# Performance work log

Measured on AMD Instinct MI355X. Metric: run time of the kernel, lower is better.

## Reference

```python
import jax, jax.numpy as jnp
import numpy as np

N = 100000   # nodes
E = 1600000  # edges
HID = 128    # hidden_dim
H = 8        # heads
C = HID // H # head_dim = out_channels per head


def setup_inputs() -> dict:
    key = jax.random.key(0)
    ks = jax.random.split(key, 10)
    x = jax.random.normal(ks[0], (N, HID), jnp.float32)
    edge_index = jax.random.randint(ks[1], (2, E), 0, N, dtype=jnp.int64)
    edge_attr = jax.random.uniform(ks[2], (E,), jnp.float32)
    # GATConv params (lin_src == lin_dst shared since in_channels is int)
    W = jax.random.normal(ks[3], (HID, H * C), jnp.float32) / np.sqrt(HID)
    att_src = jax.random.normal(ks[4], (H, C), jnp.float32) / np.sqrt(C)
    att_dst = jax.random.normal(ks[5], (H, C), jnp.float32) / np.sqrt(C)
    # lin_edge: Linear(edge_dim=1, H*C, bias=False) -> weight [H*C, 1] stored as [H, C]
    w_edge = jax.random.normal(ks[6], (H, C), jnp.float32)
    att_edge = jax.random.normal(ks[7], (H, C), jnp.float32) / np.sqrt(C)
    bias = jnp.zeros((H * C,), jnp.float32)
    gamma = jnp.ones((HID,), jnp.float32)
    beta = jnp.zeros((HID,), jnp.float32)
    return dict(x=x, edge_index=edge_index, edge_attr=edge_attr, W=W,
                att_src=att_src, att_dst=att_dst, w_edge=w_edge,
                att_edge=att_edge, bias=bias, gamma=gamma, beta=beta)


def reference(x, edge_index, edge_attr, W, att_src, att_dst, w_edge, att_edge, bias, gamma, beta):
    n = x.shape[0]
    src, dst = edge_index[0], edge_index[1]
    # add_self_loops with fill_value='mean': loop edge_attr = per-dst-node mean of edge_attr
    ones = jnp.ones_like(edge_attr)
    deg = jax.ops.segment_sum(ones, dst, num_segments=n)
    loop_attr = jax.ops.segment_sum(edge_attr, dst, num_segments=n) / jnp.maximum(deg, 1.0)
    ar = jnp.arange(n, dtype=src.dtype)
    src = jnp.concatenate([src, ar])
    dst = jnp.concatenate([dst, ar])
    ea = jnp.concatenate([edge_attr, loop_attr])  # [E+N]

    h = (x @ W).reshape(n, H, C)                  # [N,H,C]
    a_src = (h * att_src).sum(-1)                 # [N,H]
    a_dst = (h * att_dst).sum(-1)                 # [N,H]
    # edge_dim=1: alpha_edge = <lin_edge(ea), att_edge> = ea * sum(w_edge*att_edge)
    w_e = (w_edge * att_edge).sum(-1)             # [H]
    alpha = a_src[src] + a_dst[dst] + ea[:, None] * w_e  # [E+N, H]
    alpha = jax.nn.leaky_relu(alpha, 0.2)
    # segment softmax over incoming edges of each dst node (all nodes have a self-loop)
    m = jax.ops.segment_max(alpha, dst, num_segments=n)      # [N,H]
    ex = jnp.exp(alpha - m[dst])
    denom = jax.ops.segment_sum(ex, dst, num_segments=n)     # [N,H]
    p = ex / (denom[dst] + 1e-16)
    # scatter-aggregate weighted messages, concat heads, bias
    out = jax.ops.segment_sum(p[:, :, None] * h[src], dst, num_segments=n)
    out = out.reshape(n, H * C) + bias
    # residual + LayerNorm + ReLU
    y = out + x
    mu = y.mean(-1, keepdims=True)
    var = ((y - mu) ** 2).mean(-1, keepdims=True)
    y = (y - mu) * jax.lax.rsqrt(var + 1e-5) * gamma + beta
    return jax.nn.relu(y)
```

## Files before the change

### kernel.cpp

```cpp
#include <hip/hip_runtime.h>
#include <math.h>

#define HID 128
#define HEADS 8
#define CDIM 16
#define NB1 256

typedef short bf8 __attribute__((ext_vector_type(8)));
typedef float f32x4 __attribute__((ext_vector_type(4)));

__device__ __forceinline__ unsigned short f2bf(float f) {
    unsigned u = __float_as_uint(f);
    unsigned r = (u + 0x7fffu + ((u >> 16) & 1u)) >> 16;
    return (unsigned short)r;
}
__device__ __forceinline__ float bf2f(unsigned short u) {
    return __uint_as_float(((unsigned)u) << 16);
}

__global__ __launch_bounds__(256) void k_tw(const float* __restrict__ W,
                                            unsigned short* __restrict__ Wt) {
    int idx = blockIdx.x * 256 + threadIdx.x;
    int j = idx >> 7, k = idx & 127;
    Wt[idx] = f2bf(W[k * HID + j]);
}

__global__ __launch_bounds__(256) void k_hist(const int* __restrict__ dst,
                                              int* __restrict__ cntmat,
                                              int E, int per, int nbkt) {
    __shared__ int h[256];
    int t = threadIdx.x;
    h[t] = 0;
    __syncthreads();
    int b0 = blockIdx.x * per;
    int b1 = min(b0 + per, E);
    for (int e = b0 + t; e < b1; e += 256)
        atomicAdd(&h[dst[e] >> 9], 1);
    __syncthreads();
    if (t < nbkt) cntmat[t * NB1 + blockIdx.x] = h[t];
}

__global__ __launch_bounds__(256) void kscanA(const int* __restrict__ in,
                                              int* __restrict__ tmp,
                                              int* __restrict__ bsum, int M) {
    __shared__ int lds[256];
    int t = threadIdx.x;
    int base = blockIdx.x * 1024 + t * 4;
    int v[4];
#pragma unroll
    for (int i = 0; i < 4; i++) {
        int idx = base + i;
        v[i] = (idx < M) ? in[idx] : 0;
    }
    int s = v[0] + v[1] + v[2] + v[3];
    lds[t] = s;
    __syncthreads();
    for (int off = 1; off < 256; off <<= 1) {
        int xv = (t >= off) ? lds[t - off] : 0;
        __syncthreads();
        lds[t] += xv;
        __syncthreads();
    }
    int run = (t > 0) ? lds[t - 1] : 0;
#pragma unroll
    for (int i = 0; i < 4; i++) {
        int idx = base + i;
        if (idx < M) tmp[idx] = run;
        run += v[i];
    }
    if (t == 255) bsum[blockIdx.x] = lds[255];
}

__global__ __launch_bounds__(128) void kscanB(const int* __restrict__ bsum,
                                              int* __restrict__ bscan, int nb,
                                              const float* __restrict__ w_edge,
                                              const float* __restrict__ att_edge,
                                              float* __restrict__ w_e) {
    __shared__ int lds[128];
    int t = threadIdx.x;
    if (t < HEADS) {
        float s = 0.f;
        for (int c = 0; c < CDIM; c++) s += w_edge[t * CDIM + c] * att_edge[t * CDIM + c];
        w_e[t] = s;
    }
    lds[t] = (t < nb) ? bsum[t] : 0;
    __syncthreads();
    for (int off = 1; off < 128; off <<= 1) {
        int xv = (t >= off) ? lds[t - off] : 0;
        __syncthreads();
        lds[t] += xv;
        __syncthreads();
    }
    bscan[t] = (t > 0) ? lds[t - 1] : 0;
}

__global__ __launch_bounds__(256) void kscanC(const int* __restrict__ tmp,
                                              const int* __restrict__ bscan,
                                              int* __restrict__ ofs, int M) {
    int i = blockIdx.x * 256 + threadIdx.x;
    if (i < M) ofs[i] = tmp[i] + bscan[i >> 10];
}

__global__ __launch_bounds__(256) void k_scat(const int* __restrict__ src,
                                              const int* __restrict__ dst,
                                              const float* __restrict__ eattr,
                                              const int* __restrict__ ofs,
                                              int* __restrict__ d1,
                                              int2* __restrict__ erec1,
                                              int E, int per, int nbkt) {
    __shared__ int cur[256];
    int t = threadIdx.x;
    if (t < nbkt) cur[t] = ofs[t * NB1 + blockIdx.x];
    __syncthreads();
    int b0 = blockIdx.x * per;
    int b1 = min(b0 + per, E);
    for (int e = b0 + t; e < b1; e += 256) {
        int d = dst[e];
        int pos = atomicAdd(&cur[d >> 9], 1);
        d1[pos] = d;
        erec1[pos] = make_int2(src[e], __float_as_int(eattr[e]));
    }
}

__global__ __launch_bounds__(256) void k_bin(const int* __restrict__ ofs,
                                             const int* __restrict__ d1,
                                             const int2* __restrict__ erec1,
                                             int* __restrict__ row_ptr,
                                             int2* __restrict__ erec,
                                             int N, int E, int nbkt) {
    __shared__ int h2[512];
    __shared__ int s2[256];
    __shared__ int cur2[512];
    int b = blockIdx.x, t = threadIdx.x;
    int base = ofs[b * NB1];
    int end = (b + 1 < nbkt) ? ofs[(b + 1) * NB1] : E;
    h2[t] = 0; h2[t + 256] = 0;
    __syncthreads();
    for (int e = base + t; e < end; e += 256)
        atomicAdd(&h2[d1[e] & 511], 1);
    __syncthreads();
    int a0 = h2[2 * t], a1 = h2[2 * t + 1];
    s2[t] = a0 + a1;
    __syncthreads();
    for (int off = 1; off < 256; off <<= 1) {
        int v = (t >= off) ? s2[t - off] : 0;
        __syncthreads();
        s2[t] += v;
        __syncthreads();
    }
    int ex = (t > 0) ? s2[t - 1] : 0;
    int p0 = base + ex;
    int p1 = p0 + a0;
    int ng = b * 512 + 2 * t;
    if (ng <= N) row_ptr[ng] = p0;
    if (ng + 1 <= N) row_ptr[ng + 1] = p1;
    cur2[2 * t] = p0;
    cur2[2 * t + 1] = p1;
    __syncthreads();
    for (int e = base + t; e < end; e += 256) {
        int d = d1[e];
        int pos = atomicAdd(&cur2[d & 511], 1);
        erec[pos] = erec1[e];
    }
}

__global__ __launch_bounds__(256) void k_gemm(const float* __restrict__ x,
                                              const unsigned short* __restrict__ Wt,
                                              const float* __restrict__ att_src,
                                              const float* __restrict__ att_dst,
                                              unsigned short* __restrict__ hbf,
                                              float* __restrict__ a_src,
                                              float* __restrict__ a_dst, int N) {
    int tid = threadIdx.x;
    int wv = tid >> 6, lane = tid & 63;
    int nloc = lane & 15, q = lane >> 4;
    int node = blockIdx.x * 64 + wv * 16 + nloc;
    int nc = min(node, N - 1);
    const float* xp = x + (size_t)nc * HID + q * 8;
    const unsigned short* wp = Wt + nloc * HID + q * 8;
    f32x4 acc[8];
#pragma unroll
    for (int i = 0; i < 8; i++) acc[i] = (f32x4){0.f, 0.f, 0.f, 0.f};
#pragma unroll
    for (int ch = 0; ch < 4; ch++) {
        float4 xv0 = *(const float4*)(xp + ch * 32);
        float4 xv1 = *(const float4*)(xp + ch * 32 + 4);
        bf8 bfrag;
        bfrag[0] = (short)f2bf(xv0.x); bfrag[1] = (short)f2bf(xv0.y);
        bfrag[2] = (short)f2bf(xv0.z); bfrag[3] = (short)f2bf(xv0.w);
        bfrag[4] = (short)f2bf(xv1.x); bfrag[5] = (short)f2bf(xv1.y);
        bfrag[6] = (short)f2bf(xv1.z); bfrag[7] = (short)f2bf(xv1.w);
#pragma unroll
        for (int jt = 0; jt < 8; jt++) {
            bf8 afrag = *(const bf8*)(wp + (size_t)jt * 16 * HID + ch * 32);
            acc[jt] = __builtin_amdgcn_mfma_f32_16x16x32_bf16(afrag, bfrag, acc[jt], 0, 0, 0);
        }
    }
    bool ok = node < N;
    size_t hb = (size_t)nc * HID;
#pragma unroll
    for (int jt = 0; jt < 8; jt++) {
        int j0 = jt * 16 + q * 4;
        float4 as4 = *(const float4*)(att_src + j0);
        float4 ad4 = *(const float4*)(att_dst + j0);
        f32x4 a = acc[jt];
        float ps = a[0] * as4.x + a[1] * as4.y + a[2] * as4.z + a[3] * as4.w;
        float pd = a[0] * ad4.x + a[1] * ad4.y + a[2] * ad4.z + a[3] * ad4.w;
        ps += __shfl_xor(ps, 16, 64); ps += __shfl_xor(ps, 32, 64);
        pd += __shfl_xor(pd, 16, 64); pd += __shfl_xor(pd, 32, 64);
        if (ok) {
            ushort4 hv;
            hv.x = f2bf(a[0]); hv.y = f2bf(a[1]); hv.z = f2bf(a[2]); hv.w = f2bf(a[3]);
            *(ushort4*)(hbf + hb + j0) = hv;
            if (q == 0) {
                a_src[(size_t)node * 8 + jt] = ps;
                a_dst[(size_t)node * 8 + jt] = pd;
            }
        }
    }
}

__global__ __launch_bounds__(64) void k_node(const int* __restrict__ row_ptr,
                                             const int2* __restrict__ erec,
                                             const float* __restrict__ a_src,
                                             const float* __restrict__ a_dst,
                                             const float* __restrict__ w_e,
                                             const unsigned short* __restrict__ hbf,
                                             const float* __restrict__ x,
                                             const float* __restrict__ bias,
                                             const float* __restrict__ gamma,
                                             const float* __restrict__ beta,
                                             float* __restrict__ out, int N) {
    int n = blockIdx.x;
    int lane = threadIdx.x;
    int r0 = row_ptr[n], r1 = row_ptr[n + 1];
    __shared__ float lex[64][9];
    __shared__ int lsrc[64];
    float ad[8], we[8];
#pragma unroll
    for (int q = 0; q < 8; q++) {
        ad[q] = a_dst[(size_t)n * 8 + q];
        we[q] = w_e[q];
    }
    float dsum[8];
#pragma unroll
    for (int q = 0; q < 8; q++) dsum[q] = 0.f;
    float acc0 = 0.f, acc1 = 0.f;
    float suma = 0.f;
    int head = lane >> 3;

    for (int base = r0; base < r1; base += 64) {
        int e = base + lane;
        if (e < r1) {
            int2 rec = erec[e];
            int s = rec.x;
            float a = __int_as_float(rec.y);
            suma += a;
            lsrc[lane] = s;
            const float* asp = a_src + (size_t)s * 8;
#pragma unroll
            for (int q = 0; q < 8; q++) {
                float v = asp[q] + ad[q] + a * we[q];
                v = v > 0.f ? v : 0.2f * v;
                float ex = __expf(v);
                dsum[q] += ex;
                lex[lane][q] = ex;
            }
        }
        __syncthreads();
        int cntc = min(64, r1 - base);
        for (int kk = 0; kk < cntc; kk++) {
            int s = lsrc[kk];
            ushort2 hv = *(const ushort2*)(hbf + (size_t)s * HID + 2 * lane);
            float w = lex[kk][head];
            acc0 = fmaf(w, bf2f(hv.x), acc0);
            acc1 = fmaf(w, bf2f(hv.y), acc1);
        }
        __syncthreads();
    }
#pragma unroll
    for (int q = 0; q < 8; q++) {
        float v = dsum[q];
#pragma unroll
        for (int off = 32; off; off >>= 1) v += __shfl_xor(v, off, 64);
        dsum[q] = v;
    }
#pragma unroll
    for (int off = 32; off; off >>= 1) suma += __shfl_xor(suma, off, 64);

    int deg = r1 - r0;
    float la = suma / fmaxf((float)deg, 1.0f);
    float vs = a_src[(size_t)n * 8 + head] + ad[head] + la * we[head];
    vs = vs > 0.f ? vs : 0.2f * vs;
    float exs = __expf(vs);
    size_t bx = (size_t)n * HID;
    ushort2 hs = *(const ushort2*)(hbf + bx + 2 * lane);
    acc0 = fmaf(exs, bf2f(hs.x), acc0);
    acc1 = fmaf(exs, bf2f(hs.y), acc1);
    float inv = 1.f / (dsum[head] + exs + 1e-16f);

    float2 xv = *(const float2*)(x + bx + 2 * lane);
    float2 bv = *(const float2*)(bias + 2 * lane);
    float y0 = acc0 * inv + bv.x + xv.x;
    float y1 = acc1 * inv + bv.y + xv.y;
    float ss = y0 + y1, sq = y0 * y0 + y1 * y1;
#pragma unroll
    for (int off = 32; off; off >>= 1) {
        ss += __shfl_xor(ss, off, 64);
        sq += __shfl_xor(sq, off, 64);
    }
    float mu = ss * (1.f / 128.f);
    float var = sq * (1.f / 128.f) - mu * mu;
    float r = rsqrtf(fmaxf(var, 0.f) + 1e-5f);
    float2 gv = *(const float2*)(gamma + 2 * lane);
    float2 tv = *(const float2*)(beta + 2 * lane);
    float o0 = (y0 - mu) * r * gv.x + tv.x;
    float o1 = (y1 - mu) * r * gv.y + tv.y;
    float2 ov = make_float2(fmaxf(o0, 0.f), fmaxf(o1, 0.f));
    *(float2*)(out + bx + 2 * lane) = ov;
}

extern "C" void kernel_launch(void* const* d_in, const int* in_sizes, int n_in,
                              void* d_out, int out_size, void* d_ws, size_t ws_size,
                              hipStream_t stream) {
    const float* x        = (const float*)d_in[0];
    const int*   ei       = (const int*)d_in[1];
    const float* eattr    = (const float*)d_in[2];
    const float* W        = (const float*)d_in[3];
    const float* att_src  = (const float*)d_in[4];
    const float* att_dst  = (const float*)d_in[5];
    const float* w_edge   = (const float*)d_in[6];
    const float* att_edge = (const float*)d_in[7];
    const float* bias     = (const float*)d_in[8];
    const float* gamma    = (const float*)d_in[9];
    const float* beta     = (const float*)d_in[10];

    int N = in_sizes[0] / HID;
    int E = in_sizes[2];
    const int* src = ei;
    const int* dst = ei + E;
    float* out = (float*)d_out;

    int nbkt = (N + 511) >> 9;
    int M = nbkt * NB1;
    int per = (E + NB1 - 1) / NB1;

    char* ws = (char*)d_ws;
    size_t off = 0;
    auto alloc = [&](size_t bytes) { char* p = ws + off; off += (bytes + 255) & ~255ull; return p; };
    unsigned short* hbf = (unsigned short*)alloc((size_t)N * HID * 2);
    unsigned short* Wt  = (unsigned short*)alloc((size_t)HID * HID * 2);
    float* a_src   = (float*)alloc((size_t)N * 8 * 4);
    float* a_dst   = (float*)alloc((size_t)N * 8 * 4);
    int2*  erec    = (int2*) alloc((size_t)E * 8);
    int2*  erec1   = (int2*) alloc((size_t)E * 8);
    int*   d1      = (int*)  alloc((size_t)E * 4);
    int*   cntmat  = (int*)  alloc((size_t)M * 4);
    int*   stmp    = (int*)  alloc((size_t)M * 4);
    int*   ofs     = (int*)  alloc((size_t)M * 4);
    int*   bsum    = (int*)  alloc(128 * 4);
    int*   bscan   = (int*)  alloc(128 * 4);
    int*   row_ptr = (int*)  alloc((size_t)(N + 1) * 4);
    float* w_e     = (float*)alloc(8 * 4);

    int nbA = (M + 1023) / 1024;

    k_tw<<<64, 256, 0, stream>>>(W, Wt);
    k_hist<<<NB1, 256, 0, stream>>>(dst, cntmat, E, per, nbkt);
    kscanA<<<nbA, 256, 0, stream>>>(cntmat, stmp, bsum, M);
    kscanB<<<1, 128, 0, stream>>>(bsum, bscan, nbA, w_edge, att_edge, w_e);
    kscanC<<<(M + 255) / 256, 256, 0, stream>>>(stmp, bscan, ofs, M);
    k_scat<<<NB1, 256, 0, stream>>>(src, dst, eattr, ofs, d1, erec1, E, per, nbkt);
    k_bin<<<nbkt, 256, 0, stream>>>(ofs, d1, erec1, row_ptr, erec, N, E, nbkt);
    k_gemm<<<(N + 63) / 64, 256, 0, stream>>>(x, Wt, att_src, att_dst, hbf, a_src, a_dst, N);
    k_node<<<N, 64, 0, stream>>>(row_ptr, erec, a_src, a_dst, w_e, hbf, x,
                                 bias, gamma, beta, out, N);
}
```

Before: 338.1 us.

## Gather 16-byte bf16 rows across four edges per wave in node aggregation

Each wave in the per-node aggregation now handles four edges per iteration. Sixteen lanes each load a 16-byte bf16 chunk of a neighbor row, instead of all 64 lanes reading 4 bytes of a single edge's row. The softmax denominator is accumulated alongside the weighted sums, which removes the separate eight-head dsum shuffle reduction. Partial sums are combined with cross-lane shuffles and staged through shared memory before the epilogue. This is meant to cut the serial edge loop length and widen memory transactions, at the cost of more registers, zero-padding of tail edges and an extra barrier.

```diff
diff --git a/kernel.cpp b/kernel.cpp
--- a/kernel.cpp
+++ b/kernel.cpp
@@ -236,18 +236,25 @@
     int r0 = row_ptr[n], r1 = row_ptr[n + 1];
     __shared__ float lex[64][9];
     __shared__ int lsrc[64];
+    __shared__ float accs[128];
+    __shared__ float wl[16];
+
     float ad[8], we[8];
 #pragma unroll
     for (int q = 0; q < 8; q++) {
         ad[q] = a_dst[(size_t)n * 8 + q];
         we[q] = w_e[q];
     }
-    float dsum[8];
-#pragma unroll
-    for (int q = 0; q < 8; q++) dsum[q] = 0.f;
-    float acc0 = 0.f, acc1 = 0.f;
+    int sub = lane >> 4;
+    int colg = lane & 15;
+    int whead = colg >> 1;
+    const unsigned short* hbase = hbf + (size_t)colg * 8;
+
+    float acc[8];
+#pragma unroll
+    for (int j = 0; j < 8; j++) acc[j] = 0.f;
+    float wsum = 0.f;
     float suma = 0.f;
-    int head = lane >> 3;
 
     for (int base = r0; base < r1; base += 64) {
         int e = base + lane;
@@ -262,47 +269,66 @@
             for (int q = 0; q < 8; q++) {
                 float v = asp[q] + ad[q] + a * we[q];
                 v = v > 0.f ? v : 0.2f * v;
-                float ex = __expf(v);
-                dsum[q] += ex;
-                lex[lane][q] = ex;
+                lex[lane][q] = __expf(v);
             }
+        } else {
+            lsrc[lane] = 0;
+#pragma unroll
+            for (int q = 0; q < 8; q++) lex[lane][q] = 0.f;
         }
         __syncthreads();
-        int cntc = min(64, r1 - base);
-        for (int kk = 0; kk < cntc; kk++) {
-            int s = lsrc[kk];
-            ushort2 hv = *(const ushort2*)(hbf + (size_t)s * HID + 2 * lane);
-            float w = lex[kk][head];
-            acc0 = fmaf(w, bf2f(hv.x), acc0);
-            acc1 = fmaf(w, bf2f(hv.y), acc1);
+        int nt4 = (min(64, r1 - base) + 3) >> 2;
+        for (int kk = 0; kk < nt4; kk++) {
+            int ke = 4 * kk + sub;
+            int s = lsrc[ke];
+            bf8 hv = *(const bf8*)(hbase + (size_t)s * HID);
+            float w = lex[ke][whead];
+            wsum += w;
+#pragma unroll
+            for (int j = 0; j < 8; j++)
+                acc[j] = fmaf(w, bf2f((unsigned short)hv[j]), acc[j]);
         }
         __syncthreads();
     }
-#pragma unroll
-    for (int q = 0; q < 8; q++) {
-        float v = dsum[q];
-#pragma unroll
-        for (int off = 32; off; off >>= 1) v += __shfl_xor(v, off, 64);
-        dsum[q] = v;
-    }
+
+#pragma unroll
+    for (int j = 0; j < 8; j++) {
+        acc[j] += __shfl_xor(acc[j], 16, 64);
+        acc[j] += __shfl_xor(acc[j], 32, 64);
+    }
+    wsum += __shfl_xor(wsum, 16, 64);
+    wsum += __shfl_xor(wsum, 32, 64);
 #pragma unroll
     for (int off = 32; off; off >>= 1) suma += __shfl_xor(suma, off, 64);
+
+    if (lane < 16) {
+#pragma unroll
+        for (int j = 0; j < 8; j++) accs[lane * 8 + j] = acc[j];
+        wl[lane] = wsum;
+    }
+    __syncthreads();
+
+    int head = lane >> 3;
+    float denom = wl[head * 2];
+    float a0 = accs[2 * lane], a1 = accs[2 * lane + 1];
 
     int deg = r1 - r0;
     float la = suma / fmaxf((float)deg, 1.0f);
-    float vs = a_src[(size_t)n * 8 + head] + ad[head] + la * we[head];
+    float adh = a_dst[(size_t)n * 8 + head];
+    float weh = w_e[head];
+    float vs = a_src[(size_t)n * 8 + head] + adh + la * weh;
     vs = vs > 0.f ? vs : 0.2f * vs;
     float exs = __expf(vs);
     size_t bx = (size_t)n * HID;
     ushort2 hs = *(const ushort2*)(hbf + bx + 2 * lane);
-    acc0 = fmaf(exs, bf2f(hs.x), acc0);
-    acc1 = fmaf(exs, bf2f(hs.y), acc1);
-    float inv = 1.f / (dsum[head] + exs + 1e-16f);
+    a0 = fmaf(exs, bf2f(hs.x), a0);
+    a1 = fmaf(exs, bf2f(hs.y), a1);
+    float inv = 1.f / (denom + exs + 1e-16f);
 
     float2 xv = *(const float2*)(x + bx + 2 * lane);
     float2 bv = *(const float2*)(bias + 2 * lane);
-    float y0 = acc0 * inv + bv.x + xv.x;
-    float y1 = acc1 * inv + bv.y + xv.y;
+    float y0 = a0 * inv + bv.x + xv.x;
+    float y1 = a1 * inv + bv.y + xv.y;
     float ss = y0 + y1, sq = y0 * y0 + y1 * y1;
 #pragma unroll
     for (int off = 32; off; off >>= 1) {
```

Result: no change. 336.2 us (-0.6%).
